# Performance work log

Hardware: AMD Instinct MI355X
Metric: run time of the kernel (lower is better)

The kernel has to match this reference:

```python
import jax, jax.numpy as jnp
import numpy as np

HIDDEN = 768
HEADS = 12
HEAD_DIM = HIDDEN // HEADS
BETA = 0.5
BANDWIDTH = 1.0
D_INTRINSIC = 3
LN_EPS = 1e-12


def setup_inputs() -> dict:
    key = jax.random.key(0)
    ks = jax.random.split(key, 10)
    B, S, E = 2, 2048, HIDDEN
    sc = 1.0 / np.sqrt(E)
    return {
        "hidden_states": jax.random.normal(ks[0], (B, S, E), jnp.float32),
        "attention_mask": jnp.zeros((B, S), jnp.float32),
        "Wq": jax.random.normal(ks[1], (E, E), jnp.float32) * sc,
        "bq": jax.random.normal(ks[2], (E,), jnp.float32) * 0.02,
        "Wv": jax.random.normal(ks[3], (E, E), jnp.float32) * sc,
        "bv": jax.random.normal(ks[4], (E,), jnp.float32) * 0.02,
        "Wo": jax.random.normal(ks[5], (E, E), jnp.float32) * sc,
        "bo": jax.random.normal(ks[6], (E,), jnp.float32) * 0.02,
        "ln_g": jnp.ones((E,), jnp.float32),
        "ln_b": jnp.zeros((E,), jnp.float32),
    }


def _layernorm(x, g, b, eps=LN_EPS):
    mu = jnp.mean(x, axis=-1, keepdims=True)
    var = jnp.mean((x - mu) ** 2, axis=-1, keepdims=True)
    return (x - mu) * jax.lax.rsqrt(var + eps) * g + b


def reference(hidden_states, attention_mask, Wq, bq, Wv, bv, Wo, bo, ln_g, ln_b):
    B, S, E = hidden_states.shape
    H, D = HEADS, HEAD_DIM
    # projections (torch Linear: x @ W.T + b)
    q = (hidden_states @ Wq.T + bq).reshape(B, S, H, D).transpose(0, 2, 1, 3)  # [B,H,S,D]
    v = (hidden_states @ Wv.T + bv).reshape(B, S, H, D).transpose(0, 2, 1, 3)  # [B,H,S,D]
    # pairwise Euclidean distance (cdist) via norm expansion, safe sqrt
    qn = jnp.sum(q * q, axis=-1)  # [B,H,S]
    d2 = qn[:, :, :, None] + qn[:, :, None, :] - 2.0 * jnp.einsum("bhid,bhjd->bhij", q, q)
    dist = jnp.sqrt(jnp.maximum(d2, 1e-12))  # [B,H,S,S]
    # mask: positions with attention_mask < 0 get distance 2
    keep = (attention_mask >= 0)  # [B,S]
    pair_keep = keep[:, None, :, None] & keep[:, None, None, :]  # [B,1,S,S]
    dist = jnp.where(pair_keep, dist, 2.0)
    # power-law score + softmax
    attn_score = (1.0 + dist / (BANDWIDTH ** 0.5)) ** (-D_INTRINSIC - BETA)
    attn = jax.nn.softmax(attn_score, axis=-1)
    out = jnp.einsum("bhij,bhjd->bhid", attn, v)  # [B,H,S,D]
    out = out.transpose(0, 2, 1, 3).reshape(B, S, E)
    # ModelSelfOutput: dense + residual + LayerNorm (dropout=0, eval)
    out = out @ Wo.T + bo
    return _layernorm(out + hidden_states, ln_g, ln_b)
```

## Files before the change

kernel.cpp:

```cpp
#include <hip/hip_runtime.h>
#include <hip/hip_bf16.h>
#include <cstdint>
#include <cstddef>

#define S_LEN 2048
#define NH 12
#define HD 64
#define EDIM 768

typedef short bf16x8 __attribute__((ext_vector_type(8)));
typedef float f32x4  __attribute__((ext_vector_type(4)));

__device__ __forceinline__ unsigned short f2bf(float f) {
    return __bfloat16_as_ushort(__float2bfloat16(f));
}
__device__ __forceinline__ float bf2f(unsigned short u) {
    union { unsigned int i; float f; } x;
    x.i = ((unsigned int)u) << 16;
    return x.f;
}
__device__ __forceinline__ float rsq_f32(float x) {
#if __has_builtin(__builtin_amdgcn_rsqf)
    return __builtin_amdgcn_rsqf(x);
#else
    return __builtin_amdgcn_rcpf(__builtin_amdgcn_sqrtf(x));
#endif
}

__global__ __launch_bounds__(256) void precast_kernel(
    const float* __restrict__ hs, const float* __restrict__ Wq,
    const float* __restrict__ Wv, const float* __restrict__ Wo,
    unsigned short* __restrict__ hsb, unsigned short* __restrict__ Wqvb,
    unsigned short* __restrict__ Wob)
{
    const int i4 = blockIdx.x * 256 + threadIdx.x;
    const float* src;
    unsigned short* dst;
    int rel;
    if (i4 < 786432)        { src = hs; dst = hsb;            rel = i4; }
    else if (i4 < 933888)   { src = Wq; dst = Wqvb;           rel = i4 - 786432; }
    else if (i4 < 1081344)  { src = Wv; dst = Wqvb + 589824;  rel = i4 - 933888; }
    else                    { src = Wo; dst = Wob;            rel = i4 - 1081344; }
    float4 v = ((const float4*)src)[rel];
    ushort4 o;
    o.x = f2bf(v.x); o.y = f2bf(v.y); o.z = f2bf(v.z); o.w = f2bf(v.w);
    ((ushort4*)dst)[rel] = o;
}

__global__ __launch_bounds__(256) void qv_gemm(
    const unsigned short* __restrict__ hsb, const unsigned short* __restrict__ Wqvb,
    const float* __restrict__ bq, const float* __restrict__ bv,
    unsigned short* __restrict__ Qb, unsigned short* __restrict__ Vt,
    float* __restrict__ qn)
{
    __shared__ __align__(16) unsigned short As[64][40];
    __shared__ __align__(16) unsigned short Bs[128][40];

    const int t  = threadIdx.x;
    const int m0 = blockIdx.y << 6;
    const int c0 = blockIdx.x << 7;
    const bool isQ = (c0 < EDIM);
    const float* bias = isQ ? bq : bv;
    const int cb = isQ ? c0 : (c0 - EDIM);

    const int w  = t >> 6;
    const int l  = t & 63;
    const int ll = l & 15;
    const int lq = l >> 4;
    const int wx = w & 1;
    const int wy = w >> 1;

    const int srowA = t & 63;
    const int skA   = (t >> 6) << 3;
    const int srowB = t & 127;
    const int skB   = (t >> 7) << 4;

    f32x4 acc[2][4];
#pragma unroll
    for (int m = 0; m < 2; m++)
#pragma unroll
        for (int n = 0; n < 4; n++) acc[m][n] = (f32x4){0.f, 0.f, 0.f, 0.f};

    for (int k0 = 0; k0 < EDIM; k0 += 32) {
        bf16x8 va  = *(const bf16x8*)(hsb  + (size_t)(m0 + srowA) * EDIM + k0 + skA);
        bf16x8 vb0 = *(const bf16x8*)(Wqvb + (size_t)(c0 + srowB) * EDIM + k0 + skB);
        bf16x8 vb1 = *(const bf16x8*)(Wqvb + (size_t)(c0 + srowB) * EDIM + k0 + skB + 8);
        __syncthreads();
        *(bf16x8*)&As[srowA][skA]     = va;
        *(bf16x8*)&Bs[srowB][skB]     = vb0;
        *(bf16x8*)&Bs[srowB][skB + 8] = vb1;
        __syncthreads();
        bf16x8 aF[2], bF[4];
#pragma unroll
        for (int m = 0; m < 2; m++)
            aF[m] = *(const bf16x8*)&As[(wy << 5) + (m << 4) + ll][lq << 3];
#pragma unroll
        for (int n = 0; n < 4; n++)
            bF[n] = *(const bf16x8*)&Bs[(wx << 6) + (n << 4) + ll][lq << 3];
#pragma unroll
        for (int m = 0; m < 2; m++)
#pragma unroll
            for (int n = 0; n < 4; n++)
                acc[m][n] = __builtin_amdgcn_mfma_f32_16x16x32_bf16(aF[m], bF[n], acc[m][n], 0, 0, 0);
    }

    const int hcol0 = cb + (wx << 6);
    const int h = hcol0 >> 6;
    const int rowbase = m0 + (wy << 5);
    const int b = rowbase >> 11;
    const int sbase = rowbase & 2047;

    if (isQ) {
#pragma unroll
        for (int m = 0; m < 2; m++) {
#pragma unroll
            for (int r = 0; r < 4; r++) {
                const int si = sbase + (m << 4) + (lq << 2) + r;
                unsigned short* qrow = Qb + ((size_t)(b * NH + h) * S_LEN + si) * HD;
                float qsq = 0.f;
#pragma unroll
                for (int n = 0; n < 4; n++) {
                    unsigned short u = f2bf(acc[m][n][r] + bias[hcol0 + (n << 4) + ll]);
                    qrow[(n << 4) + ll] = u;
                    float f = bf2f(u);
                    qsq += f * f;
                }
                qsq += __shfl_xor(qsq, 1);
                qsq += __shfl_xor(qsq, 2);
                qsq += __shfl_xor(qsq, 4);
                qsq += __shfl_xor(qsq, 8);
                if (ll == 0) qn[(b * NH + h) * S_LEN + si] = qsq;
            }
        }
    } else {
#pragma unroll
        for (int m = 0; m < 2; m++) {
            const int si = sbase + (m << 4) + (lq << 2);
#pragma unroll
            for (int n = 0; n < 4; n++) {
                ushort4 o;
                o.x = f2bf(acc[m][n][0] + bias[hcol0 + (n << 4) + ll]);
                o.y = f2bf(acc[m][n][1] + bias[hcol0 + (n << 4) + ll]);
                o.z = f2bf(acc[m][n][2] + bias[hcol0 + (n << 4) + ll]);
                o.w = f2bf(acc[m][n][3] + bias[hcol0 + (n << 4) + ll]);
                *(ushort4*)&Vt[((size_t)(b * NH + h) * HD + (n << 4) + ll) * S_LEN + si] = o;
            }
        }
    }
}

template<int CUR>
__device__ __forceinline__ void attn_tile(
    int j0, int jn,
    const unsigned short* __restrict__ Qbase,
    const unsigned short* __restrict__ Vbase,
    const float* __restrict__ qnb, const float* __restrict__ mb,
    int ll, int lq,
    const bf16x8 (&aQ)[2][2],
    const float (&qni)[2][4], const float (&keepi)[2][4],
    const bf16x8& ones,
    f32x4 (&oacc)[2][4], f32x4 (&wacc)[2],
    bf16x8 (&nb0)[2], bf16x8 (&nb1)[2],
    bf16x8 (&vbuf)[2][4],
    unsigned short (&Wt)[2][2][16][40])
{
    constexpr int PRV = CUR ^ 1;
    __builtin_amdgcn_wave_barrier();
#pragma unroll
    for (int m = 0; m < 4; m++)
        vbuf[CUR][m] = *(const bf16x8*)(Vbase + (size_t)((m << 4) + ll) * S_LEN + j0 + (lq << 3));
    float qnjv[2], kjf[2];
#pragma unroll
    for (int n = 0; n < 2; n++) {
        int jc = j0 + (n << 4) + ll;
        qnjv[n] = qnb[jc];
        kjf[n]  = (mb[jc] >= 0.f) ? 1.f : 0.f;
    }
    f32x4 s[2][2];
#pragma unroll
    for (int s2 = 0; s2 < 2; s2++)
#pragma unroll
        for (int n = 0; n < 2; n++) {
            f32x4 c = (f32x4){0.f, 0.f, 0.f, 0.f};
            c = __builtin_amdgcn_mfma_f32_16x16x32_bf16(aQ[s2][0], nb0[n], c, 0, 0, 0);
            c = __builtin_amdgcn_mfma_f32_16x16x32_bf16(aQ[s2][1], nb1[n], c, 0, 0, 0);
            s[s2][n] = c;
        }
#pragma unroll
    for (int n = 0; n < 2; n++) {
        const unsigned short* bp = Qbase + (size_t)(jn + (n << 4) + ll) * HD + (lq << 3);
        nb0[n] = *(const bf16x8*)bp;
        nb1[n] = *(const bf16x8*)(bp + 32);
    }
#pragma unroll
    for (int s2 = 0; s2 < 2; s2++) {
        bf16x8 aP = *(const bf16x8*)&Wt[PRV][s2][ll][lq << 3];
#pragma unroll
        for (int m = 0; m < 4; m++)
            oacc[s2][m] = __builtin_amdgcn_mfma_f32_16x16x32_bf16(aP, vbuf[PRV][m], oacc[s2][m], 0, 0, 0);
        wacc[s2] = __builtin_amdgcn_mfma_f32_16x16x32_bf16(aP, ones, wacc[s2], 0, 0, 0);
    }
#pragma unroll
    for (int s2 = 0; s2 < 2; s2++)
#pragma unroll
        for (int n = 0; n < 2; n++)
#pragma unroll
            for (int r = 0; r < 4; r++) {
                float d2   = fmaf(-2.f, s[s2][n][r], qni[s2][r] + qnjv[n]);
                float dist = __builtin_amdgcn_sqrtf(fmaxf(d2, 1e-12f));
                dist = (keepi[s2][r] * kjf[n] != 0.f) ? dist : 2.0f;
                float x  = 1.0f + dist;
                float x2 = x * x;
                float x7 = x2 * x2 * x2 * x;
                float p  = rsq_f32(x7);
                float wv = fmaf(fmaf(fmaf(fmaf(0.041666668f, p, 0.16666667f),
                                          p, 0.5f), p, 1.0f), p, 1.0f);
                union { float f; unsigned int u; } cv; cv.f = wv;
                Wt[CUR][s2][(lq << 2) + r][(n << 4) + ll] =
                    (unsigned short)((cv.u + 0x8000u) >> 16);
            }
}

__global__ __launch_bounds__(64) void attn_kernel(
    const unsigned short* __restrict__ Qb, const unsigned short* __restrict__ Vt,
    const float* __restrict__ qn, const float* __restrict__ mask,
    unsigned short* __restrict__ AObf)
{
    __shared__ __align__(16) unsigned short Wt[2][2][16][40];

    const int l  = threadIdx.x;
    const int ll = l & 15;
    const int lq = l >> 4;
    const int id = blockIdx.x;
    const int ib = id / 24;
    const int bh = id - ib * 24;
    const int b  = bh / NH;
    const int h  = bh - b * NH;
    const int iw = ib << 5;

    const unsigned short* Qbase = Qb + ((size_t)bh << 17);
    const unsigned short* Vbase = Vt + ((size_t)bh << 17);
    const float* qnb = qn + (bh << 11);
    const float* mb  = mask + (b << 11);

    bf16x8 aQ[2][2];
#pragma unroll
    for (int s2 = 0; s2 < 2; s2++) {
        const unsigned short* qp = Qbase + (size_t)(iw + (s2 << 4) + ll) * HD + (lq << 3);
        aQ[s2][0] = *(const bf16x8*)qp;
        aQ[s2][1] = *(const bf16x8*)(qp + 32);
    }

    float qni[2][4], keepi[2][4];
#pragma unroll
    for (int s2 = 0; s2 < 2; s2++)
#pragma unroll
        for (int r = 0; r < 4; r++) {
            int row = iw + (s2 << 4) + (lq << 2) + r;
            qni[s2][r]   = qnb[row];
            keepi[s2][r] = (mb[row] >= 0.f) ? 1.f : 0.f;
        }

    bf16x8 ones;
#pragma unroll
    for (int i = 0; i < 8; i++) ones[i] = (short)0x3F80;

    f32x4 oacc[2][4];
#pragma unroll
    for (int s2 = 0; s2 < 2; s2++)
#pragma unroll
        for (int m = 0; m < 4; m++) oacc[s2][m] = (f32x4){0.f, 0.f, 0.f, 0.f};
    f32x4 wacc[2];
    wacc[0] = (f32x4){0.f, 0.f, 0.f, 0.f};
    wacc[1] = (f32x4){0.f, 0.f, 0.f, 0.f};

    bf16x8 nb0[2], nb1[2];
#pragma unroll
    for (int n = 0; n < 2; n++) {
        const unsigned short* bp = Qbase + (size_t)((n << 4) + ll) * HD + (lq << 3);
        nb0[n] = *(const bf16x8*)bp;
        nb1[n] = *(const bf16x8*)(bp + 32);
    }
    bf16x8 vbuf[2][4];

    {
#pragma unroll
        for (int m = 0; m < 4; m++)
            vbuf[0][m] = *(const bf16x8*)(Vbase + (size_t)((m << 4) + ll) * S_LEN + (lq << 3));
        float qnjv[2], kjf[2];
#pragma unroll
        for (int n = 0; n < 2; n++) {
            int jc = (n << 4) + ll;
            qnjv[n] = qnb[jc];
            kjf[n]  = (mb[jc] >= 0.f) ? 1.f : 0.f;
        }
        f32x4 s[2][2];
#pragma unroll
        for (int s2 = 0; s2 < 2; s2++)
#pragma unroll
            for (int n = 0; n < 2; n++) {
                f32x4 c = (f32x4){0.f, 0.f, 0.f, 0.f};
                c = __builtin_amdgcn_mfma_f32_16x16x32_bf16(aQ[s2][0], nb0[n], c, 0, 0, 0);
                c = __builtin_amdgcn_mfma_f32_16x16x32_bf16(aQ[s2][1], nb1[n], c, 0, 0, 0);
                s[s2][n] = c;
            }
#pragma unroll
        for (int n = 0; n < 2; n++) {
            const unsigned short* bp = Qbase + (size_t)(32 + (n << 4) + ll) * HD + (lq << 3);
            nb0[n] = *(const bf16x8*)bp;
            nb1[n] = *(const bf16x8*)(bp + 32);
        }
#pragma unroll
        for (int s2 = 0; s2 < 2; s2++)
#pragma unroll
            for (int n = 0; n < 2; n++)
#pragma unroll
                for (int r = 0; r < 4; r++) {
                    float d2   = fmaf(-2.f, s[s2][n][r], qni[s2][r] + qnjv[n]);
                    float dist = __builtin_amdgcn_sqrtf(fmaxf(d2, 1e-12f));
                    dist = (keepi[s2][r] * kjf[n] != 0.f) ? dist : 2.0f;
                    float x  = 1.0f + dist;
                    float x2 = x * x;
                    float x7 = x2 * x2 * x2 * x;
                    float p  = rsq_f32(x7);
                    float wv = fmaf(fmaf(fmaf(fmaf(0.041666668f, p, 0.16666667f),
                                              p, 0.5f), p, 1.0f), p, 1.0f);
                    union { float f; unsigned int u; } cv; cv.f = wv;
                    Wt[0][s2][(lq << 2) + r][(n << 4) + ll] =
                        (unsigned short)((cv.u + 0x8000u) >> 16);
                }
    }

    for (int base = 1; base <= 61; base += 2) {
        attn_tile<1>(base << 5, (base + 1) << 5, Qbase, Vbase, qnb, mb, ll, lq,
                     aQ, qni, keepi, ones, oacc, wacc, nb0, nb1, vbuf, Wt);
        attn_tile<0>((base + 1) << 5, (base + 2) << 5, Qbase, Vbase, qnb, mb, ll, lq,
                     aQ, qni, keepi, ones, oacc, wacc, nb0, nb1, vbuf, Wt);
    }
    attn_tile<1>(63 << 5, 0, Qbase, Vbase, qnb, mb, ll, lq,
                 aQ, qni, keepi, ones, oacc, wacc, nb0, nb1, vbuf, Wt);

    __builtin_amdgcn_wave_barrier();
#pragma unroll
    for (int s2 = 0; s2 < 2; s2++) {
        bf16x8 aP = *(const bf16x8*)&Wt[1][s2][ll][lq << 3];
#pragma unroll
        for (int m = 0; m < 4; m++)
            oacc[s2][m] = __builtin_amdgcn_mfma_f32_16x16x32_bf16(aP, vbuf[1][m], oacc[s2][m], 0, 0, 0);
        wacc[s2] = __builtin_amdgcn_mfma_f32_16x16x32_bf16(aP, ones, wacc[s2], 0, 0, 0);
    }

#pragma unroll
    for (int s2 = 0; s2 < 2; s2++)
#pragma unroll
        for (int r = 0; r < 4; r++) {
            float inv = 1.0f / wacc[s2][r];
            const int row = iw + (s2 << 4) + (lq << 2) + r;
            unsigned short* dst = AObf + (size_t)((b << 11) + row) * EDIM + (h << 6);
#pragma unroll
            for (int m = 0; m < 4; m++)
                dst[(m << 4) + ll] = f2bf(oacc[s2][m][r] * inv);
        }
}

__global__ __launch_bounds__(256) void oproj_gemm(
    const unsigned short* __restrict__ AObf, const unsigned short* __restrict__ Wob,
    const float* __restrict__ bo, const float* __restrict__ hs,
    float* __restrict__ TMP)
{
    __shared__ __align__(16) unsigned short As[64][40];
    __shared__ __align__(16) unsigned short Bs[64][40];

    const int t  = threadIdx.x;
    const int m0 = blockIdx.y << 6;
    const int c0 = blockIdx.x << 6;

    const int w  = t >> 6;
    const int l  = t & 63;
    const int ll = l & 15;
    const int lq = l >> 4;
    const int wx = w & 1;
    const int wy = w >> 1;

    const int srow = t & 63;
    const int sk   = (t >> 6) << 3;

    f32x4 acc[2][2];
#pragma unroll
    for (int m = 0; m < 2; m++)
#pragma unroll
        for (int n = 0; n < 2; n++) acc[m][n] = (f32x4){0.f, 0.f, 0.f, 0.f};

    for (int k0 = 0; k0 < EDIM; k0 += 32) {
        bf16x8 va = *(const bf16x8*)(AObf + (size_t)(m0 + srow) * EDIM + k0 + sk);
        bf16x8 vb = *(const bf16x8*)(Wob  + (size_t)(c0 + srow) * EDIM + k0 + sk);
        __syncthreads();
        *(bf16x8*)&As[srow][sk] = va;
        *(bf16x8*)&Bs[srow][sk] = vb;
        __syncthreads();
        bf16x8 aF[2], bF[2];
#pragma unroll
        for (int m = 0; m < 2; m++)
            aF[m] = *(const bf16x8*)&As[(wy << 5) + (m << 4) + ll][lq << 3];
#pragma unroll
        for (int n = 0; n < 2; n++)
            bF[n] = *(const bf16x8*)&Bs[(wx << 5) + (n << 4) + ll][lq << 3];
#pragma unroll
        for (int m = 0; m < 2; m++)
#pragma unroll
            for (int n = 0; n < 2; n++)
                acc[m][n] = __builtin_amdgcn_mfma_f32_16x16x32_bf16(aF[m], bF[n], acc[m][n], 0, 0, 0);
    }

#pragma unroll
    for (int m = 0; m < 2; m++) {
#pragma unroll
        for (int r = 0; r < 4; r++) {
            const int row = m0 + (wy << 5) + (m << 4) + (lq << 2) + r;
#pragma unroll
            for (int n = 0; n < 2; n++) {
                const int col = c0 + (wx << 5) + (n << 4) + ll;
                TMP[(size_t)row * EDIM + col] =
                    acc[m][n][r] + bo[col] + hs[(size_t)row * EDIM + col];
            }
        }
    }
}

__global__ __launch_bounds__(256) void ln_kernel(
    const float* __restrict__ X, const float* __restrict__ g,
    const float* __restrict__ be, float* __restrict__ out)
{
    const int row = blockIdx.x;
    const int t = threadIdx.x;
    const float* x = X + (size_t)row * EDIM;

    float s = 0.f, sq = 0.f;
#pragma unroll
    for (int c = t; c < EDIM; c += 256) {
        float v = x[c];
        s += v; sq += v * v;
    }
#pragma unroll
    for (int m = 1; m < 64; m <<= 1) {
        s  += __shfl_xor(s, m);
        sq += __shfl_xor(sq, m);
    }
    __shared__ float ss[4], ssq[4];
    const int w = t >> 6;
    if ((t & 63) == 0) { ss[w] = s; ssq[w] = sq; }
    __syncthreads();
    s  = ss[0] + ss[1] + ss[2] + ss[3];
    sq = ssq[0] + ssq[1] + ssq[2] + ssq[3];
    const float mu  = s * (1.f / EDIM);
    const float var = sq * (1.f / EDIM) - mu * mu;
    const float rstd = 1.0f / sqrtf(var + 1e-12f);

#pragma unroll
    for (int c = t; c < EDIM; c += 256) {
        out[(size_t)row * EDIM + c] = (x[c] - mu) * rstd * g[c] + be[c];
    }
}

extern "C" void kernel_launch(void* const* d_in, const int* in_sizes, int n_in,
                              void* d_out, int out_size, void* d_ws, size_t ws_size,
                              hipStream_t stream) {
    const float* hs   = (const float*)d_in[0];
    const float* mask = (const float*)d_in[1];
    const float* Wq   = (const float*)d_in[2];
    const float* bq   = (const float*)d_in[3];
    const float* Wv   = (const float*)d_in[4];
    const float* bv   = (const float*)d_in[5];
    const float* Wo   = (const float*)d_in[6];
    const float* bo   = (const float*)d_in[7];
    const float* g    = (const float*)d_in[8];
    const float* be   = (const float*)d_in[9];

    char* w8 = (char*)d_ws;
    unsigned short* Qb   = (unsigned short*)(w8);
    unsigned short* Vt   = (unsigned short*)(w8 +  6291456);
    float*          qn   = (float*)        (w8 + 12582912);
    unsigned short* AObf = (unsigned short*)(w8 + 12779520);
    unsigned short* hsb  = (unsigned short*)(w8 + 19070976);
    unsigned short* Wqvb = (unsigned short*)(w8 + 25362432);
    unsigned short* Wob  = (unsigned short*)(w8 + 27721728);
    float*          TMP  = (float*)(w8);

    precast_kernel<<<dim3(4800),    256, 0, stream>>>(hs, Wq, Wv, Wo, hsb, Wqvb, Wob);
    qv_gemm       <<<dim3(12, 64),  256, 0, stream>>>(hsb, Wqvb, bq, bv, Qb, Vt, qn);
    attn_kernel   <<<dim3(1536),    64,  0, stream>>>(Qb, Vt, qn, mask, AObf);
    oproj_gemm    <<<dim3(12, 64),  256, 0, stream>>>(AObf, Wob, bo, hs, TMP);
    ln_kernel     <<<dim3(4096),    256, 0, stream>>>(TMP, g, be, (float*)d_out);
}
```

Baseline: 262.0 us.

## Split attention key loop across four waves with shared-memory reduction

The attention kernel now launches 256 threads per block, and each of the four waves processes a quarter of the key tiles for the same 32 query rows. Partial output accumulators and row weight sums are reduced through shared memory in two stages before wave 0 normalizes and writes the result. The aim is more waves in flight and a shorter serial loop per wave, improving latency hiding. The cost is redundant Q fragment loads per wave, extra LDS use and several block barriers for the reduction.

Result: slower. 335.4 us (+28.0%).

```diff
diff --git a/kernel.cpp b/kernel.cpp
--- a/kernel.cpp
+++ b/kernel.cpp
@@ -221,14 +221,16 @@
             }
 }
 
-__global__ __launch_bounds__(64) void attn_kernel(
+__global__ __launch_bounds__(256, 4) void attn_kernel(
     const unsigned short* __restrict__ Qb, const unsigned short* __restrict__ Vt,
     const float* __restrict__ qn, const float* __restrict__ mask,
     unsigned short* __restrict__ AObf)
 {
-    __shared__ __align__(16) unsigned short Wt[2][2][16][40];
-
-    const int l  = threadIdx.x;
+    __shared__ __align__(16) unsigned short Wt[4][2][2][16][40];
+
+    const int t  = threadIdx.x;
+    const int w  = t >> 6;
+    const int l  = t & 63;
     const int ll = l & 15;
     const int lq = l >> 4;
     const int id = blockIdx.x;
@@ -243,6 +245,11 @@
     const float* qnb = qn + (bh << 11);
     const float* mb  = mask + (b << 11);
 
+    unsigned short (&Wtw)[2][2][16][40] = Wt[w];
+
+    const int tbase = w << 4;
+    const int jb    = tbase << 5;
+
     bf16x8 aQ[2][2];
 #pragma unroll
     for (int s2 = 0; s2 < 2; s2++) {
@@ -277,7 +284,7 @@
     bf16x8 nb0[2], nb1[2];
 #pragma unroll
     for (int n = 0; n < 2; n++) {
-        const unsigned short* bp = Qbase + (size_t)((n << 4) + ll) * HD + (lq << 3);
+        const unsigned short* bp = Qbase + (size_t)(jb + (n << 4) + ll) * HD + (lq << 3);
         nb0[n] = *(const bf16x8*)bp;
         nb1[n] = *(const bf16x8*)(bp + 32);
     }
@@ -286,11 +293,11 @@
     {
 #pragma unroll
         for (int m = 0; m < 4; m++)
-            vbuf[0][m] = *(const bf16x8*)(Vbase + (size_t)((m << 4) + ll) * S_LEN + (lq << 3));
+            vbuf[0][m] = *(const bf16x8*)(Vbase + (size_t)((m << 4) + ll) * S_LEN + jb + (lq << 3));
         float qnjv[2], kjf[2];
 #pragma unroll
         for (int n = 0; n < 2; n++) {
-            int jc = (n << 4) + ll;
+            int jc = jb + (n << 4) + ll;
             qnjv[n] = qnb[jc];
             kjf[n]  = (mb[jc] >= 0.f) ? 1.f : 0.f;
         }
@@ -306,7 +313,7 @@
             }
 #pragma unroll
         for (int n = 0; n < 2; n++) {
-            const unsigned short* bp = Qbase + (size_t)(32 + (n << 4) + ll) * HD + (lq << 3);
+            const unsigned short* bp = Qbase + (size_t)(jb + 32 + (n << 4) + ll) * HD + (lq << 3);
             nb0[n] = *(const bf16x8*)bp;
             nb1[n] = *(const bf16x8*)(bp + 32);
         }
@@ -326,41 +333,107 @@
                     float wv = fmaf(fmaf(fmaf(fmaf(0.041666668f, p, 0.16666667f),
                                               p, 0.5f), p, 1.0f), p, 1.0f);
                     union { float f; unsigned int u; } cv; cv.f = wv;
-                    Wt[0][s2][(lq << 2) + r][(n << 4) + ll] =
+                    Wtw[0][s2][(lq << 2) + r][(n << 4) + ll] =
                         (unsigned short)((cv.u + 0x8000u) >> 16);
                 }
     }
 
-    for (int base = 1; base <= 61; base += 2) {
-        attn_tile<1>(base << 5, (base + 1) << 5, Qbase, Vbase, qnb, mb, ll, lq,
-                     aQ, qni, keepi, ones, oacc, wacc, nb0, nb1, vbuf, Wt);
-        attn_tile<0>((base + 1) << 5, (base + 2) << 5, Qbase, Vbase, qnb, mb, ll, lq,
-                     aQ, qni, keepi, ones, oacc, wacc, nb0, nb1, vbuf, Wt);
-    }
-    attn_tile<1>(63 << 5, 0, Qbase, Vbase, qnb, mb, ll, lq,
-                 aQ, qni, keepi, ones, oacc, wacc, nb0, nb1, vbuf, Wt);
+    for (int tt = tbase + 1; tt <= tbase + 13; tt += 2) {
+        attn_tile<1>(tt << 5, (tt + 1) << 5, Qbase, Vbase, qnb, mb, ll, lq,
+                     aQ, qni, keepi, ones, oacc, wacc, nb0, nb1, vbuf, Wtw);
+        attn_tile<0>((tt + 1) << 5, (tt + 2) << 5, Qbase, Vbase, qnb, mb, ll, lq,
+                     aQ, qni, keepi, ones, oacc, wacc, nb0, nb1, vbuf, Wtw);
+    }
+    attn_tile<1>((tbase + 15) << 5, 0, Qbase, Vbase, qnb, mb, ll, lq,
+                 aQ, qni, keepi, ones, oacc, wacc, nb0, nb1, vbuf, Wtw);
 
     __builtin_amdgcn_wave_barrier();
 #pragma unroll
     for (int s2 = 0; s2 < 2; s2++) {
-        bf16x8 aP = *(const bf16x8*)&Wt[1][s2][ll][lq << 3];
+        bf16x8 aP = *(const bf16x8*)&Wtw[1][s2][ll][lq << 3];
 #pragma unroll
         for (int m = 0; m < 4; m++)
             oacc[s2][m] = __builtin_amdgcn_mfma_f32_16x16x32_bf16(aP, vbuf[1][m], oacc[s2][m], 0, 0, 0);
         wacc[s2] = __builtin_amdgcn_mfma_f32_16x16x32_bf16(aP, ones, wacc[s2], 0, 0, 0);
     }
 
-#pragma unroll
-    for (int s2 = 0; s2 < 2; s2++)
-#pragma unroll
-        for (int r = 0; r < 4; r++) {
-            float inv = 1.0f / wacc[s2][r];
-            const int row = iw + (s2 << 4) + (lq << 2) + r;
-            unsigned short* dst = AObf + (size_t)((b << 11) + row) * EDIM + (h << 6);
+    float* red = (float*)Wt;
+    __syncthreads();
+    if (w >= 2) {
+        float* p = red + (((w - 2) << 6) + l);
+#pragma unroll
+        for (int s2 = 0; s2 < 2; s2++)
 #pragma unroll
             for (int m = 0; m < 4; m++)
-                dst[(m << 4) + ll] = f2bf(oacc[s2][m][r] * inv);
-        }
+#pragma unroll
+                for (int r = 0; r < 4; r++)
+                    p[((((s2 << 2) + m) << 2) + r) * 128] = oacc[s2][m][r];
+#pragma unroll
+        for (int s2 = 0; s2 < 2; s2++)
+#pragma unroll
+            for (int r = 0; r < 4; r++)
+                p[(32 + (s2 << 2) + r) * 128] = wacc[s2][r];
+    }
+    __syncthreads();
+    if (w < 2) {
+        float* p = red + ((w << 6) + l);
+#pragma unroll
+        for (int s2 = 0; s2 < 2; s2++)
+#pragma unroll
+            for (int m = 0; m < 4; m++)
+#pragma unroll
+                for (int r = 0; r < 4; r++)
+                    oacc[s2][m][r] += p[((((s2 << 2) + m) << 2) + r) * 128];
+#pragma unroll
+        for (int s2 = 0; s2 < 2; s2++)
+#pragma unroll
+            for (int r = 0; r < 4; r++)
+                wacc[s2][r] += p[(32 + (s2 << 2) + r) * 128];
+    }
+    __syncthreads();
+    if (w == 1) {
+        float* p = red + l;
+#pragma unroll
+        for (int s2 = 0; s2 < 2; s2++)
+#pragma unroll
+            for (int m = 0; m < 4; m++)
+#pragma unroll
+                for (int r = 0; r < 4; r++)
+                    p[((((s2 << 2) + m) << 2) + r) * 128] = oacc[s2][m][r];
+#pragma unroll
+        for (int s2 = 0; s2 < 2; s2++)
+#pragma unroll
+            for (int r = 0; r < 4; r++)
+                p[(32 + (s2 << 2) + r) * 128] = wacc[s2][r];
+    }
+    __syncthreads();
+    if (w == 0) {
+        float* p = red + l;
+#pragma unroll
+        for (int s2 = 0; s2 < 2; s2++)
+#pragma unroll
+            for (int m = 0; m < 4; m++)
+#pragma unroll
+                for (int r = 0; r < 4; r++)
+                    oacc[s2][m][r] += p[((((s2 << 2) + m) << 2) + r) * 128];
+#pragma unroll
+        for (int s2 = 0; s2 < 2; s2++)
+#pragma unroll
+            for (int r = 0; r < 4; r++)
+                wacc[s2][r] += p[(32 + (s2 << 2) + r) * 128];
+
+#pragma unroll
+        for (int s2 = 0; s2 < 2; s2++)
+#pragma unroll
+            for (int r = 0; r < 4; r++) {
+                float inv = 1.0f / wacc[s2][r];
+                const int row = iw + (s2 << 4) + (lq << 2) + r;
+                unsigned short* dst = AObf + (size_t)((b << 11) + row) * EDIM + (h << 6);
+#pragma unroll
+                for (int m = 0; m < 4; m++)
+                    dst[(m << 4) + ll] = f2bf(oacc[s2][m][r] * inv);
+            }
+    }
 }
 
 __global__ __launch_bounds__(256) void oproj_gemm(
@@ -488,7 +561,7 @@
 
     precast_kernel<<<dim3(4800),    256, 0, stream>>>(hs, Wq, Wv, Wo, hsb, Wqvb, Wob);
     qv_gemm       <<<dim3(12, 64),  256, 0, stream>>>(hsb, Wqvb, bq, bv, Qb, Vt, qn);
-    attn_kernel   <<<dim3(1536),    64,  0, stream>>>(Qb, Vt, qn, mask, AObf);
+    attn_kernel   <<<dim3(1536),    256, 0, stream>>>(Qb, Vt, qn, mask, AObf);
     oproj_gemm    <<<dim3(12, 64),  256, 0, stream>>>(AObf, Wob, bo, hs, TMP);
     ln_kernel     <<<dim3(4096),    256, 0, stream>>>(TMP, g, be, (float*)d_out);
 }
```

## Halve attention query tile to 16 rows per wave, doubling grid size

Applied to the files above, without the earlier changes.

Each attention wave now handles 16 query rows instead of 32, so the grid doubles to 3072 single-wave blocks. This lowers per-wave register and LDS use and adds more waves to hide latency. In exchange, every Q/V key tile is loaded twice as often across the grid. The key norms and mask values are now prefetched one tile ahead, and the score math is written in two-wide float vectors with the mask applied through an FMA instead of a select, which may allow packed FP32 instructions.

Result: slower. 333.3 us (+27.2%).

```diff
diff --git a/kernel.cpp b/kernel.cpp
--- a/kernel.cpp
+++ b/kernel.cpp
@@ -10,6 +10,7 @@
 
 typedef short bf16x8 __attribute__((ext_vector_type(8)));
 typedef float f32x4  __attribute__((ext_vector_type(4)));
+typedef float f32x2  __attribute__((ext_vector_type(2)));
 
 __device__ __forceinline__ unsigned short f2bf(float f) {
     return __bfloat16_as_ushort(__float2bfloat16(f));
@@ -150,75 +151,80 @@
 }
 
 template<int CUR>
-__device__ __forceinline__ void attn_tile(
+__device__ __forceinline__ void attn_tile16(
     int j0, int jn,
     const unsigned short* __restrict__ Qbase,
     const unsigned short* __restrict__ Vbase,
     const float* __restrict__ qnb, const float* __restrict__ mb,
     int ll, int lq,
-    const bf16x8 (&aQ)[2][2],
-    const float (&qni)[2][4], const float (&keepi)[2][4],
+    const bf16x8 (&aQ)[2],
+    const f32x2 (&qni2)[2], const f32x2 (&keepi2)[2],
     const bf16x8& ones,
-    f32x4 (&oacc)[2][4], f32x4 (&wacc)[2],
+    f32x4 (&oacc)[4], f32x4& wacc,
     bf16x8 (&nb0)[2], bf16x8 (&nb1)[2],
     bf16x8 (&vbuf)[2][4],
-    unsigned short (&Wt)[2][2][16][40])
+    float (&qnjv)[2][2], float (&kjm)[2][2],
+    unsigned short (&Wt)[2][16][40])
 {
     constexpr int PRV = CUR ^ 1;
     __builtin_amdgcn_wave_barrier();
 #pragma unroll
     for (int m = 0; m < 4; m++)
         vbuf[CUR][m] = *(const bf16x8*)(Vbase + (size_t)((m << 4) + ll) * S_LEN + j0 + (lq << 3));
-    float qnjv[2], kjf[2];
+    f32x4 s[2];
 #pragma unroll
     for (int n = 0; n < 2; n++) {
-        int jc = j0 + (n << 4) + ll;
-        qnjv[n] = qnb[jc];
-        kjf[n]  = (mb[jc] >= 0.f) ? 1.f : 0.f;
-    }
-    f32x4 s[2][2];
-#pragma unroll
-    for (int s2 = 0; s2 < 2; s2++)
-#pragma unroll
-        for (int n = 0; n < 2; n++) {
-            f32x4 c = (f32x4){0.f, 0.f, 0.f, 0.f};
-            c = __builtin_amdgcn_mfma_f32_16x16x32_bf16(aQ[s2][0], nb0[n], c, 0, 0, 0);
-            c = __builtin_amdgcn_mfma_f32_16x16x32_bf16(aQ[s2][1], nb1[n], c, 0, 0, 0);
-            s[s2][n] = c;
-        }
+        f32x4 c = (f32x4){0.f, 0.f, 0.f, 0.f};
+        c = __builtin_amdgcn_mfma_f32_16x16x32_bf16(aQ[0], nb0[n], c, 0, 0, 0);
+        c = __builtin_amdgcn_mfma_f32_16x16x32_bf16(aQ[1], nb1[n], c, 0, 0, 0);
+        s[n] = c;
+    }
 #pragma unroll
     for (int n = 0; n < 2; n++) {
         const unsigned short* bp = Qbase + (size_t)(jn + (n << 4) + ll) * HD + (lq << 3);
         nb0[n] = *(const bf16x8*)bp;
         nb1[n] = *(const bf16x8*)(bp + 32);
-    }
-#pragma unroll
-    for (int s2 = 0; s2 < 2; s2++) {
-        bf16x8 aP = *(const bf16x8*)&Wt[PRV][s2][ll][lq << 3];
+        int jc = jn + (n << 4) + ll;
+        qnjv[PRV][n] = qnb[jc];
+        kjm[PRV][n]  = (mb[jc] >= 0.f) ? 1.f : 0.f;
+    }
+    {
+        bf16x8 aP = *(const bf16x8*)&Wt[PRV][ll][lq << 3];
 #pragma unroll
         for (int m = 0; m < 4; m++)
-            oacc[s2][m] = __builtin_amdgcn_mfma_f32_16x16x32_bf16(aP, vbuf[PRV][m], oacc[s2][m], 0, 0, 0);
-        wacc[s2] = __builtin_amdgcn_mfma_f32_16x16x32_bf16(aP, ones, wacc[s2], 0, 0, 0);
-    }
-#pragma unroll
-    for (int s2 = 0; s2 < 2; s2++)
-#pragma unroll
-        for (int n = 0; n < 2; n++)
-#pragma unroll
-            for (int r = 0; r < 4; r++) {
-                float d2   = fmaf(-2.f, s[s2][n][r], qni[s2][r] + qnjv[n]);
-                float dist = __builtin_amdgcn_sqrtf(fmaxf(d2, 1e-12f));
-                dist = (keepi[s2][r] * kjf[n] != 0.f) ? dist : 2.0f;
-                float x  = 1.0f + dist;
-                float x2 = x * x;
-                float x7 = x2 * x2 * x2 * x;
-                float p  = rsq_f32(x7);
-                float wv = fmaf(fmaf(fmaf(fmaf(0.041666668f, p, 0.16666667f),
-                                          p, 0.5f), p, 1.0f), p, 1.0f);
-                union { float f; unsigned int u; } cv; cv.f = wv;
-                Wt[CUR][s2][(lq << 2) + r][(n << 4) + ll] =
-                    (unsigned short)((cv.u + 0x8000u) >> 16);
-            }
+            oacc[m] = __builtin_amdgcn_mfma_f32_16x16x32_bf16(aP, vbuf[PRV][m], oacc[m], 0, 0, 0);
+        wacc = __builtin_amdgcn_mfma_f32_16x16x32_bf16(aP, ones, wacc, 0, 0, 0);
+    }
+#pragma unroll
+    for (int n = 0; n < 2; n++) {
+        const f32x2 qv = (f32x2)(qnjv[CUR][n]);
+        const f32x2 kj = (f32x2)(kjm[CUR][n]);
+#pragma unroll
+        for (int pr = 0; pr < 2; pr++) {
+            f32x2 sp = { s[n][2*pr], s[n][2*pr + 1] };
+            f32x2 d2 = __builtin_elementwise_fma(sp, (f32x2)(-2.f), qni2[pr] + qv);
+            d2 = __builtin_elementwise_max(d2, (f32x2)(1e-12f));
+            f32x2 dist = { __builtin_amdgcn_sqrtf(d2.x), __builtin_amdgcn_sqrtf(d2.y) };
+            f32x2 km = keepi2[pr] * kj;
+            f32x2 x  = __builtin_elementwise_fma(km, dist + (f32x2)(-2.f), (f32x2)(3.f));
+            f32x2 x2 = x * x;
+            f32x2 x4 = x2 * x2;
+            f32x2 x6 = x4 * x2;
+            f32x2 x7 = x6 * x;
+            f32x2 p  = { rsq_f32(x7.x), rsq_f32(x7.y) };
+            f32x2 wv = __builtin_elementwise_fma(
+                __builtin_elementwise_fma(
+                    __builtin_elementwise_fma(
+                        __builtin_elementwise_fma((f32x2)(0.041666668f), p, (f32x2)(0.16666667f)),
+                        p, (f32x2)(0.5f)),
+                    p, (f32x2)(1.0f)),
+                p, (f32x2)(1.0f));
+            union { float f; unsigned int u; } c0, c1;
+            c0.f = wv.x; c1.f = wv.y;
+            Wt[CUR][(lq << 2) + 2*pr    ][(n << 4) + ll] = (unsigned short)((c0.u + 0x8000u) >> 16);
+            Wt[CUR][(lq << 2) + 2*pr + 1][(n << 4) + ll] = (unsigned short)((c1.u + 0x8000u) >> 16);
+        }
+    }
 }
 
 __global__ __launch_bounds__(64) void attn_kernel(
@@ -226,7 +232,7 @@
     const float* __restrict__ qn, const float* __restrict__ mask,
     unsigned short* __restrict__ AObf)
 {
-    __shared__ __align__(16) unsigned short Wt[2][2][16][40];
+    __shared__ __align__(16) unsigned short Wt[2][16][40];
 
     const int l  = threadIdx.x;
     const int ll = l & 15;
@@ -236,50 +242,48 @@
     const int bh = id - ib * 24;
     const int b  = bh / NH;
     const int h  = bh - b * NH;
-    const int iw = ib << 5;
+    const int iw = ib << 4;
 
     const unsigned short* Qbase = Qb + ((size_t)bh << 17);
     const unsigned short* Vbase = Vt + ((size_t)bh << 17);
     const float* qnb = qn + (bh << 11);
     const float* mb  = mask + (b << 11);
 
-    bf16x8 aQ[2][2];
-#pragma unroll
-    for (int s2 = 0; s2 < 2; s2++) {
-        const unsigned short* qp = Qbase + (size_t)(iw + (s2 << 4) + ll) * HD + (lq << 3);
-        aQ[s2][0] = *(const bf16x8*)qp;
-        aQ[s2][1] = *(const bf16x8*)(qp + 32);
-    }
-
-    float qni[2][4], keepi[2][4];
-#pragma unroll
-    for (int s2 = 0; s2 < 2; s2++)
-#pragma unroll
-        for (int r = 0; r < 4; r++) {
-            int row = iw + (s2 << 4) + (lq << 2) + r;
-            qni[s2][r]   = qnb[row];
-            keepi[s2][r] = (mb[row] >= 0.f) ? 1.f : 0.f;
-        }
+    bf16x8 aQ[2];
+    {
+        const unsigned short* qp = Qbase + (size_t)(iw + ll) * HD + (lq << 3);
+        aQ[0] = *(const bf16x8*)qp;
+        aQ[1] = *(const bf16x8*)(qp + 32);
+    }
+
+    f32x2 qni2[2], keepi2[2];
+#pragma unroll
+    for (int pr = 0; pr < 2; pr++) {
+        int r0 = iw + (lq << 2) + 2*pr;
+        qni2[pr]   = (f32x2){ qnb[r0], qnb[r0 + 1] };
+        keepi2[pr] = (f32x2){ (mb[r0] >= 0.f) ? 1.f : 0.f,
+                              (mb[r0 + 1] >= 0.f) ? 1.f : 0.f };
+    }
 
     bf16x8 ones;
 #pragma unroll
     for (int i = 0; i < 8; i++) ones[i] = (short)0x3F80;
 
-    f32x4 oacc[2][4];
-#pragma unroll
-    for (int s2 = 0; s2 < 2; s2++)
-#pragma unroll
-        for (int m = 0; m < 4; m++) oacc[s2][m] = (f32x4){0.f, 0.f, 0.f, 0.f};
-    f32x4 wacc[2];
-    wacc[0] = (f32x4){0.f, 0.f, 0.f, 0.f};
-    wacc[1] = (f32x4){0.f, 0.f, 0.f, 0.f};
+    f32x4 oacc[4];
+#pragma unroll
+    for (int m = 0; m < 4; m++) oacc[m] = (f32x4){0.f, 0.f, 0.f, 0.f};
+    f32x4 wacc = (f32x4){0.f, 0.f, 0.f, 0.f};
 
     bf16x8 nb0[2], nb1[2];
+    float qnjv[2][2], kjm[2][2];
 #pragma unroll
     for (int n = 0; n < 2; n++) {
         const unsigned short* bp = Qbase + (size_t)((n << 4) + ll) * HD + (lq << 3);
         nb0[n] = *(const bf16x8*)bp;
         nb1[n] = *(const bf16x8*)(bp + 32);
+        int jc = (n << 4) + ll;
+        qnjv[0][n] = qnb[jc];
+        kjm[0][n]  = (mb[jc] >= 0.f) ? 1.f : 0.f;
     }
     bf16x8 vbuf[2][4];
 
@@ -287,80 +291,82 @@
 #pragma unroll
         for (int m = 0; m < 4; m++)
             vbuf[0][m] = *(const bf16x8*)(Vbase + (size_t)((m << 4) + ll) * S_LEN + (lq << 3));
-        float qnjv[2], kjf[2];
+        f32x4 s[2];
 #pragma unroll
         for (int n = 0; n < 2; n++) {
-            int jc = (n << 4) + ll;
-            qnjv[n] = qnb[jc];
-            kjf[n]  = (mb[jc] >= 0.f) ? 1.f : 0.f;
-        }
-        f32x4 s[2][2];
-#pragma unroll
-        for (int s2 = 0; s2 < 2; s2++)
-#pragma unroll
-            for (int n = 0; n < 2; n++) {
-                f32x4 c = (f32x4){0.f, 0.f, 0.f, 0.f};
-                c = __builtin_amdgcn_mfma_f32_16x16x32_bf16(aQ[s2][0], nb0[n], c, 0, 0, 0);
-                c = __builtin_amdgcn_mfma_f32_16x16x32_bf16(aQ[s2][1], nb1[n], c, 0, 0, 0);
-                s[s2][n] = c;
-            }
+            f32x4 c = (f32x4){0.f, 0.f, 0.f, 0.f};
+            c = __builtin_amdgcn_mfma_f32_16x16x32_bf16(aQ[0], nb0[n], c, 0, 0, 0);
+            c = __builtin_amdgcn_mfma_f32_16x16x32_bf16(aQ[1], nb1[n], c, 0, 0, 0);
+            s[n] = c;
+        }
 #pragma unroll
         for (int n = 0; n < 2; n++) {
             const unsigned short* bp = Qbase + (size_t)(32 + (n << 4) + ll) * HD + (lq << 3);
             nb0[n] = *(const bf16x8*)bp;
             nb1[n] = *(const bf16x8*)(bp + 32);
-        }
-#pragma unroll
-        for (int s2 = 0; s2 < 2; s2++)
-#pragma unroll
-            for (int n = 0; n < 2; n++)
-#pragma unroll
-                for (int r = 0; r < 4; r++) {
-                    float d2   = fmaf(-2.f, s[s2][n][r], qni[s2][r] + qnjv[n]);
-                    float dist = __builtin_amdgcn_sqrtf(fmaxf(d2, 1e-12f));
-                    dist = (keepi[s2][r] * kjf[n] != 0.f) ? dist : 2.0f;
-                    float x  = 1.0f + dist;
-                    float x2 = x * x;
-                    float x7 = x2 * x2 * x2 * x;
-                    float p  = rsq_f32(x7);
-                    float wv = fmaf(fmaf(fmaf(fmaf(0.041666668f, p, 0.16666667f),
-                                              p, 0.5f), p, 1.0f), p, 1.0f);
-                    union { float f; unsigned int u; } cv; cv.f = wv;
-                    Wt[0][s2][(lq << 2) + r][(n << 4) + ll] =
-                        (unsigned short)((cv.u + 0x8000u) >> 16);
-                }
-    }
-
-    for (int base = 1; base <= 61; base += 2) {
-        attn_tile<1>(base << 5, (base + 1) << 5, Qbase, Vbase, qnb, mb, ll, lq,
-                     aQ, qni, keepi, ones, oacc, wacc, nb0, nb1, vbuf, Wt);
-        attn_tile<0>((base + 1) << 5, (base + 2) << 5, Qbase, Vbase, qnb, mb, ll, lq,
-                     aQ, qni, keepi, ones, oacc, wacc, nb0, nb1, vbuf, Wt);
-    }
-    attn_tile<1>(63 << 5, 0, Qbase, Vbase, qnb, mb, ll, lq,
-                 aQ, qni, keepi, ones, oacc, wacc, nb0, nb1, vbuf, Wt);
+            int jc = 32 + (n << 4) + ll;
+            qnjv[1][n] = qnb[jc];
+            kjm[1][n]  = (mb[jc] >= 0.f) ? 1.f : 0.f;
+        }
+#pragma unroll
+        for (int n = 0; n < 2; n++) {
+            const f32x2 qv = (f32x2)(qnjv[0][n]);
+            const f32x2 kj = (f32x2)(kjm[0][n]);
+#pragma unroll
+            for (int pr = 0; pr < 2; pr++) {
+                f32x2 sp = { s[n][2*pr], s[n][2*pr + 1] };
+                f32x2 d2 = __builtin_elementwise_fma(sp, (f32x2)(-2.f), qni2[pr] + qv);
+                d2 = __builtin_elementwise_max(d2, (f32x2)(1e-12f));
+                f32x2 dist = { __builtin_amdgcn_sqrtf(d2.x), __builtin_amdgcn_sqrtf(d2.y) };
+                f32x2 km = keepi2[pr] * kj;
+                f32x2 x  = __builtin_elementwise_fma(km, dist + (f32x2)(-2.f), (f32x2)(3.f));
+                f32x2 x2 = x * x;
+                f32x2 x4 = x2 * x2;
+                f32x2 x6 = x4 * x2;
+                f32x2 x7 = x6 * x;
+                f32x2 p  = { rsq_f32(x7.x), rsq_f32(x7.y) };
+                f32x2 wv = __builtin_elementwise_fma(
+                    __builtin_elementwise_fma(
+                        __builtin_elementwise_fma(
+                            __builtin_elementwise_fma((f32x2)(0.041666668f), p, (f32x2)(0.16666667f)),
+                            p, (f32x2)(0.5f)),
+                        p, (f32x2)(1.0f)),
+                    p, (f32x2)(1.0f));
+                union { float f; unsigned int u; } c0, c1;
+                c0.f = wv.x; c1.f = wv.y;
+                Wt[0][(lq << 2) + 2*pr    ][(n << 4) + ll] = (unsigned short)((c0.u + 0x8000u) >> 16);
+                Wt[0][(lq << 2) + 2*pr + 1][(n << 4) + ll] = (unsigned short)((c1.u + 0x8000u) >> 16);
+            }
+        }
+    }
+
+    for (int tt = 1; tt <= 61; tt += 2) {
+        attn_tile16<1>(tt << 5, (tt + 1) << 5, Qbase, Vbase, qnb, mb, ll, lq,
+                       aQ, qni2, keepi2, ones, oacc, wacc, nb0, nb1, vbuf, qnjv, kjm, Wt);
+        attn_tile16<0>((tt + 1) << 5, (tt + 2) << 5, Qbase, Vbase, qnb, mb, ll, lq,
+                       aQ, qni2, keepi2, ones, oacc, wacc, nb0, nb1, vbuf, qnjv, kjm, Wt);
+    }
+    attn_tile16<1>(63 << 5, 0, Qbase, Vbase, qnb, mb, ll, lq,
+                   aQ, qni2, keepi2, ones, oacc, wacc, nb0, nb1, vbuf, qnjv, kjm, Wt);
 
     __builtin_amdgcn_wave_barrier();
-#pragma unroll
-    for (int s2 = 0; s2 < 2; s2++) {
-        bf16x8 aP = *(const bf16x8*)&Wt[1][s2][ll][lq << 3];
+    {
+        bf16x8 aP = *(const bf16x8*)&Wt[1][ll][lq << 3];
 #pragma unroll
         for (int m = 0; m < 4; m++)
-            oacc[s2][m] = __builtin_amdgcn_mfma_f32_16x16x32_bf16(aP, vbuf[1][m], oacc[s2][m], 0, 0, 0);
-        wacc[s2] = __builtin_amdgcn_mfma_f32_16x16x32_bf16(aP, ones, wacc[s2], 0, 0, 0);
-    }
-
-#pragma unroll
-    for (int s2 = 0; s2 < 2; s2++)
-#pragma unroll
-        for (int r = 0; r < 4; r++) {
-            float inv = 1.0f / wacc[s2][r];
-            const int row = iw + (s2 << 4) + (lq << 2) + r;
-            unsigned short* dst = AObf + (size_t)((b << 11) + row) * EDIM + (h << 6);
-#pragma unroll
-            for (int m = 0; m < 4; m++)
-                dst[(m << 4) + ll] = f2bf(oacc[s2][m][r] * inv);
-        }
+            oacc[m] = __builtin_amdgcn_mfma_f32_16x16x32_bf16(aP, vbuf[1][m], oacc[m], 0, 0, 0);
+        wacc = __builtin_amdgcn_mfma_f32_16x16x32_bf16(aP, ones, wacc, 0, 0, 0);
+    }
+
+#pragma unroll
+    for (int r = 0; r < 4; r++) {
+        float inv = 1.0f / wacc[r];
+        const int row = iw + (lq << 2) + r;
+        unsigned short* dst = AObf + (size_t)((b << 11) + row) * EDIM + (h << 6);
+#pragma unroll
+        for (int m = 0; m < 4; m++)
+            dst[(m << 4) + ll] = f2bf(oacc[m][r] * inv);
+    }
 }
 
 __global__ __launch_bounds__(256) void oproj_gemm(
@@ -488,7 +494,7 @@
 
     precast_kernel<<<dim3(4800),    256, 0, stream>>>(hs, Wq, Wv, Wo, hsb, Wqvb, Wob);
     qv_gemm       <<<dim3(12, 64),  256, 0, stream>>>(hsb, Wqvb, bq, bv, Qb, Vt, qn);
-    attn_kernel   <<<dim3(1536),    64,  0, stream>>>(Qb, Vt, qn, mask, AObf);
+    attn_kernel   <<<dim3(3072),    64,  0, stream>>>(Qb, Vt, qn, mask, AObf);
     oproj_gemm    <<<dim3(12, 64),  256, 0, stream>>>(AObf, Wob, bo, hs, TMP);
     ln_kernel     <<<dim3(4096),    256, 0, stream>>>(TMP, g, be, (float*)d_out);
 }
```
